# Kernel optimization log

Hardware: AMD Instinct MI355X
Metric: run time of the kernel (lower is better)

## Reference

```python
import jax, jax.numpy as jnp
import numpy as np

T, B, H, IN = 2048, 4096, 51, 2

def setup_inputs() -> dict:
    key = jax.random.key(0)
    ks = jax.random.split(key, 12)
    s = 1.0 / np.sqrt(H)
    u = lambda k, shape: jax.random.uniform(k, shape, jnp.float32, -s, s)
    return {
        "input": jax.random.normal(ks[0], (T, B, IN), jnp.float32),
        "W_ih1": u(ks[1], (4 * H, IN)),
        "W_hh1": u(ks[2], (4 * H, H)),
        "b_ih1": u(ks[3], (4 * H,)),
        "b_hh1": u(ks[4], (4 * H,)),
        "W_ih2": u(ks[5], (4 * H, H)),
        "W_hh2": u(ks[6], (4 * H, H)),
        "b_ih2": u(ks[7], (4 * H,)),
        "b_hh2": u(ks[8], (4 * H,)),
        "W_lin": u(ks[9], (1, H)),
        "b_lin": u(ks[10], (1,)),
    }

def _lstm_cell(x, h, c, W_ih, W_hh, b_ih, b_hh):
    # PyTorch LSTMCell gate order: input, forget, cell(g), output
    gates = x @ W_ih.T + b_ih + h @ W_hh.T + b_hh  # [B, 4H]
    i, f, g, o = jnp.split(gates, 4, axis=-1)
    c_new = jax.nn.sigmoid(f) * c + jax.nn.sigmoid(i) * jnp.tanh(g)
    h_new = jax.nn.sigmoid(o) * jnp.tanh(c_new)
    return h_new, c_new

def reference(input, W_ih1, W_hh1, b_ih1, b_hh1, W_ih2, W_hh2, b_ih2, b_hh2, W_lin, b_lin):
    Bsz = input.shape[1]
    z = jnp.zeros((Bsz, H), input.dtype)

    def step(carry, x_t):
        h1, c1, h2, c2 = carry
        h1, c1 = _lstm_cell(x_t, h1, c1, W_ih1, W_hh1, b_ih1, b_hh1)
        h2, c2 = _lstm_cell(h1, h2, c2, W_ih2, W_hh2, b_ih2, b_hh2)
        out = h2 @ W_lin.T + b_lin  # [B, 1]
        return (h1, c1, h2, c2), out[:, 0]

    _, outs = jax.lax.scan(step, (z, z, z, z), input)  # outs: [T, B]
    return outs.T  # [B, T] == torch.stack(outputs, 1).squeeze(2)
```

## Files before the change

### kernel.cpp

```cpp
#include <hip/hip_runtime.h>

namespace {
constexpr int T    = 2048;
constexpr int Bsz  = 4096;
constexpr int H    = 51;
constexpr int H4   = 204;
constexpr int NB   = 16;
constexpr int BLK  = 1024;
constexpr int GRID = Bsz / NB;
constexpr float SCI = -1.44269504f;
constexpr float SCG = -2.88539008f;
}

typedef float    f32x4 __attribute__((ext_vector_type(4)));
typedef _Float16 f16x8 __attribute__((ext_vector_type(8)));
typedef unsigned short u16;

__device__ __forceinline__ float RCP(float x)  { return __builtin_amdgcn_rcpf(x); }
__device__ __forceinline__ float EXP2(float x) { return __builtin_amdgcn_exp2f(x); }

__device__ __forceinline__ float lstm_act(float Gi, float Gf, float Gg, float Go, float& c) {
  float ei = EXP2(Gi);
  float ef = EXP2(Gf);
  float eo = EXP2(Go);
  float eg = EXP2(-fabsf(Gg));
  float pi = 1.0f + ei, pf = 1.0f + ef, pg = 1.0f + eg;
  float tg = copysignf(1.0f - eg, -Gg);
  float pig = pi * pg;
  float num = fmaf(c, pig, tg * pf);
  c = num * RCP(pig * pf);
  float ec = EXP2(SCG * fabsf(c));
  float tc = copysignf(1.0f - ec, c);
  return tc * RCP((1.0f + eo) * (1.0f + ec));
}


__global__ __launch_bounds__(BLK, 4) void lstm2_v5(
    const float* __restrict__ x,
    const float* __restrict__ Wih1, const float* __restrict__ Whh1,
    const float* __restrict__ bih1, const float* __restrict__ bhh1,
    const float* __restrict__ Wih2, const float* __restrict__ Whh2,
    const float* __restrict__ bih2, const float* __restrict__ bhh2,
    const float* __restrict__ Wlin, const float* __restrict__ blin,
    float* __restrict__ out) {
  __shared__ __align__(16) float  SW[H4 * H];
  __shared__ __align__(16) u16    PL[4096];
  __shared__ __align__(16) float2 XB[2][32][16];
  __shared__ __align__(16) float  OB[2][16][33];

  const int tid  = threadIdx.x;
  const int lane = tid & 63;
  const int wid  = tid >> 6;
  const int a    = lane & 15;
  const int q    = lane >> 4;
  const int b0   = blockIdx.x * NB;
  const int lt   = tid - 768;

  const int  l1t    = (wid <= 12) ? wid : -1;
  const int  l2t    = (wid < 12) ? wid : ((wid == 13) ? 12 : -1);
  const bool isHead = (wid == 14);
  const bool isXinj = (wid == 15);

  f16x8 wA1[2];
  f16x8 wA2[4];
  f16x8 hA[2][2];

  for (int i = tid; i < H4 * H; i += BLK) SW[i] = Whh1[i];
  __syncthreads();
  if (l1t >= 0) {
    const int  rp   = 16 * l1t + a;
    const bool vld  = (rp < H4);
    const int  gate = rp & 3;
    const int  wrow = gate * H + (rp >> 2);
    const float sc  = (gate == 2) ? SCG : SCI;
#pragma unroll
    for (int sp = 0; sp < 2; ++sp)
#pragma unroll
      for (int j = 0; j < 8; ++j) {
        const int k = 32 * sp + 16 * (j >> 2) + 4 * q + (j & 3);
        float val = 0.f;
        if (vld) {
          if (k < H)           val = SW[wrow * H + k];
          else if (k == H)     val = Wih1[wrow * 2 + 0];
          else if (k == H + 1) val = Wih1[wrow * 2 + 1];
          else if (k == H + 2) val = bih1[wrow] + bhh1[wrow];
        }
        wA1[sp][j] = (_Float16)(val * sc);
      }
  }
  __syncthreads();
  for (int i = tid; i < H4 * H; i += BLK) SW[i] = Wih2[i];
  __syncthreads();
  if (l2t >= 0) {
    const int  rp   = 16 * l2t + a;
    const bool vld  = (rp < H4);
    const int  gate = rp & 3;
    const int  wrow = gate * H + (rp >> 2);
    const float sc  = (gate == 2) ? SCG : SCI;
#pragma unroll
    for (int sp = 0; sp < 2; ++sp)
#pragma unroll
      for (int j = 0; j < 8; ++j) {
        const int k = 32 * sp + 16 * (j >> 2) + 4 * q + (j & 3);
        float val = 0.f;
        if (vld) {
          if (k < H)           val = SW[wrow * H + k];
          else if (k == H + 2) val = bih2[wrow] + bhh2[wrow];
        }
        wA2[sp][j] = (_Float16)(val * sc);
      }
  }
  __syncthreads();
  for (int i = tid; i < H4 * H; i += BLK) SW[i] = Whh2[i];
  __syncthreads();
  if (l2t >= 0) {
    const int  rp   = 16 * l2t + a;
    const bool vld  = (rp < H4);
    const int  gate = rp & 3;
    const int  wrow = gate * H + (rp >> 2);
    const float sc  = (gate == 2) ? SCG : SCI;
#pragma unroll
    for (int sp = 2; sp < 4; ++sp)
#pragma unroll
      for (int j = 0; j < 8; ++j) {
        const int kp = 32 * (sp - 2) + 16 * (j >> 2) + 4 * q + (j & 3);
        float val = (vld && kp < H) ? SW[wrow * H + kp] * sc : 0.f;
        wA2[sp][j] = (_Float16)val;
      }
  }
  if (isHead) {
#pragma unroll
    for (int sp = 0; sp < 2; ++sp)
#pragma unroll
      for (int j = 0; j < 8; ++j) {
        const int kp = 32 * sp + 16 * (j >> 2) + 4 * q + (j & 3);
        float val = 0.f;
        if (a == 0) {
          if (kp < H)           val = Wlin[kp];
          else if (kp == H + 2) val = blin[0];
        }
        const _Float16 hi = (_Float16)val;
        hA[sp][0][j] = hi;
        hA[sp][1][j] = (_Float16)(val - (float)hi);
      }
  }

  __syncthreads();
  for (int i = tid; i < 4096; i += BLK) PL[i] = 0;
  __syncthreads();
  if (tid < 16) {
#pragma unroll
    for (int buf = 0; buf < 2; ++buf) {
      PL[(buf * 4 + 1) * 512 + (tid + 16) * 8 + 5] = 0x3C00;
      PL[(buf * 4 + 3) * 512 + (tid + 16) * 8 + 5] = 0x3C00;
    }
  }
  if (lt >= 0) {
    const int st = lt >> 3, bc = (lt & 7) * 2;
    *(float4*)&XB[0][st][bc] = *(const float4*)(x + ((size_t)st * Bsz + b0 + bc) * 2);
  }
  __syncthreads();
  if (isXinj && lane < 32) {
    const int bb = lane & 15, f = lane >> 4;
    const float xv = ((const float*)&XB[0][0][0])[bb * 2 + f];
    const int idx = 512 + ((f == 0) ? bb * 8 + 7 : (bb + 16) * 8 + 4);
    *(_Float16*)&PL[idx] = (_Float16)xv;
  }
  __syncthreads();

  int wbase1 = 0, wbase2 = 0;
  bool uval1 = false, uval2 = false;
  if (l1t >= 0) {
    const int u = 4 * l1t + q; uval1 = (u < H);
    const int spl = u >> 5, kl = u & 31;
    wbase1 = spl * 512 + (a + 16 * ((kl >> 2) & 3)) * 8 + ((kl & 3) + 4 * (kl >> 4));
  }
  if (l2t >= 0) {
    const int u = 4 * l2t + q; uval2 = (u < H);
    const int spl = u >> 5, kl = u & 31;
    wbase2 = 1024 + spl * 512 + (a + 16 * ((kl >> 2) & 3)) * 8 + ((kl & 3) + 4 * (kl >> 4));
  }

  float c1 = 0.f, c2 = 0.f;
  float4 xcr = {0.f, 0.f, 0.f, 0.f};

  for (int s = 0; s < T + 3; ++s) {
    const int pb   = (s & 1) * 2048;
    const int nbuf = 2048 - pb;

    f16x8 bh0, bh1, bh2, bh3;
    if (l1t >= 0 || l2t >= 0) {
      bh0 = *(const f16x8*)&PL[pb + lane * 8];
      bh1 = *(const f16x8*)&PL[pb + 512 + lane * 8];
    }
    if (l2t >= 0 || isHead) {
      bh2 = *(const f16x8*)&PL[pb + 1024 + lane * 8];
      bh3 = *(const f16x8*)&PL[pb + 1536 + lane * 8];
    }

    if (lt >= 0) {
      const int ph = s & 31;
      if (ph == 0) {
        if (s + 32 < T) {
          const int st = lt >> 3, bc = (lt & 7) * 2;
          xcr = *(const float4*)(x + ((size_t)(s + 32 + st) * Bsz + b0 + bc) * 2);
        }
      } else if (ph == 1) {
        if (s + 31 < T) {
          const int buf = ((s >> 5) + 1) & 1;
          const int st = lt >> 3, bc = (lt & 7) * 2;
          *(float4*)&XB[buf][st][bc] = xcr;
        }
      } else if (ph == 2 && s >= 34) {
        const int f = (s - 34) >> 5;
        const int row = lt >> 4, c0 = (lt & 15) * 2;
        const float2 v = *(const float2*)&OB[f & 1][row][c0];
        *(float2*)(out + (size_t)(b0 + row) * T + f * 32 + c0) = v;
      }
    }

    f32x4 d1, d2;
    if (l1t >= 0) {
      f32x4 acc = {0.f, 0.f, 0.f, 0.f};
      acc = __builtin_amdgcn_mfma_f32_16x16x32_f16(wA1[0], bh0, acc, 0, 0, 0);
      acc = __builtin_amdgcn_mfma_f32_16x16x32_f16(wA1[1], bh1, acc, 0, 0, 0);
      d1 = acc;
    }
    if (l2t >= 0) {
      f32x4 acc = {0.f, 0.f, 0.f, 0.f};
      acc = __builtin_amdgcn_mfma_f32_16x16x32_f16(wA2[0], bh0, acc, 0, 0, 0);
      acc = __builtin_amdgcn_mfma_f32_16x16x32_f16(wA2[1], bh1, acc, 0, 0, 0);
      acc = __builtin_amdgcn_mfma_f32_16x16x32_f16(wA2[2], bh2, acc, 0, 0, 0);
      acc = __builtin_amdgcn_mfma_f32_16x16x32_f16(wA2[3], bh3, acc, 0, 0, 0);
      d2 = acc;
    }

    if (l1t >= 0 && s < T) {
      const float h1 = lstm_act(d1[0], d1[1], d1[2], d1[3], c1);
      if (uval1) *(_Float16*)&PL[nbuf + wbase1] = (_Float16)h1;
    }
    if (l2t >= 0 && s >= 1 && s <= T) {
      const float h2 = lstm_act(d2[0], d2[1], d2[2], d2[3], c2);
      if (uval2) *(_Float16*)&PL[nbuf + wbase2] = (_Float16)h2;
    }

    if (isHead) {
      f32x4 dh = {0.f, 0.f, 0.f, 0.f};
      dh = __builtin_amdgcn_mfma_f32_16x16x32_f16(hA[0][0], bh2, dh, 0, 0, 0);
      dh = __builtin_amdgcn_mfma_f32_16x16x32_f16(hA[0][1], bh2, dh, 0, 0, 0);
      dh = __builtin_amdgcn_mfma_f32_16x16x32_f16(hA[1][0], bh3, dh, 0, 0, 0);
      dh = __builtin_amdgcn_mfma_f32_16x16x32_f16(hA[1][1], bh3, dh, 0, 0, 0);
      if (s >= 2 && s - 2 < T && lane < 16)
        OB[((s - 2) >> 5) & 1][lane][(s - 2) & 31] = dh[0];
    }
    if (isXinj && lane < 32 && s + 1 < T) {
      const int bb = lane & 15, f = lane >> 4;
      const int st = (s + 1) & 31, cb = ((s + 1) >> 5) & 1;
      const float xv = ((const float*)&XB[cb][st][0])[bb * 2 + f];
      const int idx = nbuf + 512 + ((f == 0) ? bb * 8 + 7 : (bb + 16) * 8 + 4);
      *(_Float16*)&PL[idx] = (_Float16)xv;
    }
    __syncthreads();
  }
}

extern "C" void kernel_launch(void* const* d_in, const int* in_sizes, int n_in,
                              void* d_out, int out_size, void* d_ws, size_t ws_size,
                              hipStream_t stream) {
  (void)in_sizes; (void)n_in; (void)d_ws; (void)ws_size; (void)out_size;
  const float* x    = (const float*)d_in[0];
  const float* Wih1 = (const float*)d_in[1];
  const float* Whh1 = (const float*)d_in[2];
  const float* bih1 = (const float*)d_in[3];
  const float* bhh1 = (const float*)d_in[4];
  const float* Wih2 = (const float*)d_in[5];
  const float* Whh2 = (const float*)d_in[6];
  const float* bih2 = (const float*)d_in[7];
  const float* bhh2 = (const float*)d_in[8];
  const float* Wlin = (const float*)d_in[9];
  const float* blin = (const float*)d_in[10];
  float* out = (float*)d_out;

  hipLaunchKernelGGL(lstm2_v5, dim3(GRID), dim3(BLK), 0, stream,
                     x, Wih1, Whh1, bih1, bhh1, Wih2, Whh2, bih2, bhh2,
                     Wlin, blin, out);
}
```

Baseline: 1.360 ms.

## Halve batch per block and pack two gate tiles per wave with DPP select

Each block now handles 8 batch rows with 512 threads and 8 waves instead of 16 rows with 1024 threads. Each wave computes two 16-row gate tiles and uses a DPP row select to merge the valid 8-column halves. The head projection, x staging and output writeback move into one special wave, and the head drops its fp16 hi/lo split to a single fp16 weight. Role assignment is rotated per block to balance MFMA load across SIMDs. This doubles the grid and MFMA work per useful output column, trading denser per-step barriers for more redundant matrix work and slightly lower head precision.

```diff
diff --git a/kernel.cpp b/kernel.cpp
--- a/kernel.cpp
+++ b/kernel.cpp
@@ -5,8 +5,8 @@
 constexpr int Bsz  = 4096;
 constexpr int H    = 51;
 constexpr int H4   = 204;
-constexpr int NB   = 16;
-constexpr int BLK  = 1024;
+constexpr int NB   = 8;
+constexpr int BLK  = 512;
 constexpr int GRID = Bsz / NB;
 constexpr float SCI = -1.44269504f;
 constexpr float SCG = -2.88539008f;
@@ -34,8 +34,13 @@
   return tc * RCP((1.0f + eo) * (1.0f + ec));
 }
 
-
-__global__ __launch_bounds__(BLK, 4) void lstm2_v5(
+__device__ __forceinline__ float dpp_sel(float dA, float dB) {
+  return __uint_as_float((unsigned)__builtin_amdgcn_update_dpp(
+      (int)__float_as_uint(dA), (int)__float_as_uint(dB), 0x118, 0xf, 0xf, false));
+}
+
+
+__global__ __launch_bounds__(BLK, 4) void lstm2_v6(
     const float* __restrict__ x,
     const float* __restrict__ Wih1, const float* __restrict__ Whh1,
     const float* __restrict__ bih1, const float* __restrict__ bhh1,
@@ -45,8 +50,8 @@
     float* __restrict__ out) {
   __shared__ __align__(16) float  SW[H4 * H];
   __shared__ __align__(16) u16    PL[4096];
-  __shared__ __align__(16) float2 XB[2][32][16];
-  __shared__ __align__(16) float  OB[2][16][33];
+  __shared__ __align__(16) float4 XB4[2][32][4];
+  __shared__ __align__(16) float  OB[2][8][36];
 
   const int tid  = threadIdx.x;
   const int lane = tid & 63;
@@ -54,81 +59,94 @@
   const int a    = lane & 15;
   const int q    = lane >> 4;
   const int b0   = blockIdx.x * NB;
-  const int lt   = tid - 768;
-
-  const int  l1t    = (wid <= 12) ? wid : -1;
-  const int  l2t    = (wid < 12) ? wid : ((wid == 13) ? 12 : -1);
-  const bool isHead = (wid == 14);
-  const bool isXinj = (wid == 15);
-
-  f16x8 wA1[2];
-  f16x8 wA2[4];
-  f16x8 hA[2][2];
+
+  const int role = (wid + ((blockIdx.x & 1) << 1)) & 7;
+  int l1A = -1, l1B = -1, l2A = -1, l2B = -1;
+  bool isSpec = false;
+  if (role < 6)       { l1A = 2 * role; l1B = l1A + 1; l2A = l1A; l2B = l1B; }
+  else if (role == 6) { l1A = 12; }
+  else                { l2A = 12; isSpec = true; }
+
+  f16x8 wA1[2][2];
+  f16x8 wA2[2][4];
+  f16x8 hA[2];
 
   for (int i = tid; i < H4 * H; i += BLK) SW[i] = Whh1[i];
   __syncthreads();
-  if (l1t >= 0) {
-    const int  rp   = 16 * l1t + a;
-    const bool vld  = (rp < H4);
-    const int  gate = rp & 3;
-    const int  wrow = gate * H + (rp >> 2);
-    const float sc  = (gate == 2) ? SCG : SCI;
-#pragma unroll
-    for (int sp = 0; sp < 2; ++sp)
-#pragma unroll
-      for (int j = 0; j < 8; ++j) {
-        const int k = 32 * sp + 16 * (j >> 2) + 4 * q + (j & 3);
-        float val = 0.f;
-        if (vld) {
-          if (k < H)           val = SW[wrow * H + k];
-          else if (k == H)     val = Wih1[wrow * 2 + 0];
-          else if (k == H + 1) val = Wih1[wrow * 2 + 1];
-          else if (k == H + 2) val = bih1[wrow] + bhh1[wrow];
-        }
-        wA1[sp][j] = (_Float16)(val * sc);
-      }
+#pragma unroll
+  for (int ti = 0; ti < 2; ++ti) {
+    const int t = ti ? l1B : l1A;
+    if (t >= 0) {
+      const int  rp   = 16 * t + a;
+      const bool vld  = (rp < H4);
+      const int  gate = rp & 3;
+      const int  wrow = gate * H + (rp >> 2);
+      const float sc  = (gate == 2) ? SCG : SCI;
+#pragma unroll
+      for (int sp = 0; sp < 2; ++sp)
+#pragma unroll
+        for (int j = 0; j < 8; ++j) {
+          const int k = 32 * sp + 16 * (j >> 2) + 4 * q + (j & 3);
+          float val = 0.f;
+          if (vld) {
+            if (k < H)           val = SW[wrow * H + k];
+            else if (k == H)     val = Wih1[wrow * 2 + 0];
+            else if (k == H + 1) val = Wih1[wrow * 2 + 1];
+            else if (k == H + 2) val = bih1[wrow] + bhh1[wrow];
+          }
+          wA1[ti][sp][j] = (_Float16)(val * sc);
+        }
+    }
   }
   __syncthreads();
   for (int i = tid; i < H4 * H; i += BLK) SW[i] = Wih2[i];
   __syncthreads();
-  if (l2t >= 0) {
-    const int  rp   = 16 * l2t + a;
-    const bool vld  = (rp < H4);
-    const int  gate = rp & 3;
-    const int  wrow = gate * H + (rp >> 2);
-    const float sc  = (gate == 2) ? SCG : SCI;
-#pragma unroll
-    for (int sp = 0; sp < 2; ++sp)
-#pragma unroll
-      for (int j = 0; j < 8; ++j) {
-        const int k = 32 * sp + 16 * (j >> 2) + 4 * q + (j & 3);
-        float val = 0.f;
-        if (vld) {
-          if (k < H)           val = SW[wrow * H + k];
-          else if (k == H + 2) val = bih2[wrow] + bhh2[wrow];
-        }
-        wA2[sp][j] = (_Float16)(val * sc);
-      }
+#pragma unroll
+  for (int ti = 0; ti < 2; ++ti) {
+    const int t = ti ? l2B : l2A;
+    if (t >= 0) {
+      const int  rp   = 16 * t + a;
+      const bool vld  = (rp < H4);
+      const int  gate = rp & 3;
+      const int  wrow = gate * H + (rp >> 2);
+      const float sc  = (gate == 2) ? SCG : SCI;
+#pragma unroll
+      for (int sp = 0; sp < 2; ++sp)
+#pragma unroll
+        for (int j = 0; j < 8; ++j) {
+          const int k = 32 * sp + 16 * (j >> 2) + 4 * q + (j & 3);
+          float val = 0.f;
+          if (vld) {
+            if (k < H)           val = SW[wrow * H + k];
+            else if (k == H + 2) val = bih2[wrow] + bhh2[wrow];
+          }
+          wA2[ti][sp][j] = (_Float16)(val * sc);
+        }
+    }
   }
   __syncthreads();
   for (int i = tid; i < H4 * H; i += BLK) SW[i] = Whh2[i];
   __syncthreads();
-  if (l2t >= 0) {
-    const int  rp   = 16 * l2t + a;
-    const bool vld  = (rp < H4);
-    const int  gate = rp & 3;
-    const int  wrow = gate * H + (rp >> 2);
-    const float sc  = (gate == 2) ? SCG : SCI;
-#pragma unroll
-    for (int sp = 2; sp < 4; ++sp)
-#pragma unroll
-      for (int j = 0; j < 8; ++j) {
-        const int kp = 32 * (sp - 2) + 16 * (j >> 2) + 4 * q + (j & 3);
-        float val = (vld && kp < H) ? SW[wrow * H + kp] * sc : 0.f;
-        wA2[sp][j] = (_Float16)val;
-      }
-  }
-  if (isHead) {
+#pragma unroll
+  for (int ti = 0; ti < 2; ++ti) {
+    const int t = ti ? l2B : l2A;
+    if (t >= 0) {
+      const int  rp   = 16 * t + a;
+      const bool vld  = (rp < H4);
+      const int  gate = rp & 3;
+      const int  wrow = gate * H + (rp >> 2);
+      const float sc  = (gate == 2) ? SCG : SCI;
+#pragma unroll
+      for (int sp = 2; sp < 4; ++sp)
+#pragma unroll
+        for (int j = 0; j < 8; ++j) {
+          const int kp = 32 * (sp - 2) + 16 * (j >> 2) + 4 * q + (j & 3);
+          float val = (vld && kp < H) ? SW[wrow * H + kp] * sc : 0.f;
+          wA2[ti][sp][j] = (_Float16)val;
+        }
+    }
+  }
+  if (isSpec) {
 #pragma unroll
     for (int sp = 0; sp < 2; ++sp)
 #pragma unroll
@@ -139,14 +157,16 @@
           if (kp < H)           val = Wlin[kp];
           else if (kp == H + 2) val = blin[0];
         }
-        const _Float16 hi = (_Float16)val;
-        hA[sp][0][j] = hi;
-        hA[sp][1][j] = (_Float16)(val - (float)hi);
+        hA[sp][j] = (_Float16)val;
       }
   }
 
   __syncthreads();
   for (int i = tid; i < 4096; i += BLK) PL[i] = 0;
+  if (tid < 128) {
+    const int st = tid >> 2, v4 = tid & 3;
+    XB4[0][st][v4] = *(const float4*)(x + ((size_t)st * Bsz + b0) * 2 + v4 * 4);
+  }
   __syncthreads();
   if (tid < 16) {
 #pragma unroll
@@ -155,110 +175,142 @@
       PL[(buf * 4 + 3) * 512 + (tid + 16) * 8 + 5] = 0x3C00;
     }
   }
-  if (lt >= 0) {
-    const int st = lt >> 3, bc = (lt & 7) * 2;
-    *(float4*)&XB[0][st][bc] = *(const float4*)(x + ((size_t)st * Bsz + b0 + bc) * 2);
-  }
-  __syncthreads();
-  if (isXinj && lane < 32) {
-    const int bb = lane & 15, f = lane >> 4;
-    const float xv = ((const float*)&XB[0][0][0])[bb * 2 + f];
+  __syncthreads();
+  if (isSpec && lane < 16) {
+    const int bb = lane & 7, f = (lane >> 3) & 1;
+    const float xv = ((const float*)&XB4[0][0][0])[bb * 2 + f];
     const int idx = 512 + ((f == 0) ? bb * 8 + 7 : (bb + 16) * 8 + 4);
     *(_Float16*)&PL[idx] = (_Float16)xv;
   }
   __syncthreads();
 
-  int wbase1 = 0, wbase2 = 0;
+  int widx1 = 0, widx2 = 0;
   bool uval1 = false, uval2 = false;
-  if (l1t >= 0) {
-    const int u = 4 * l1t + q; uval1 = (u < H);
-    const int spl = u >> 5, kl = u & 31;
-    wbase1 = spl * 512 + (a + 16 * ((kl >> 2) & 3)) * 8 + ((kl & 3) + 4 * (kl >> 4));
-  }
-  if (l2t >= 0) {
-    const int u = 4 * l2t + q; uval2 = (u < H);
-    const int spl = u >> 5, kl = u & 31;
-    wbase2 = 1024 + spl * 512 + (a + 16 * ((kl >> 2) & 3)) * 8 + ((kl & 3) + 4 * (kl >> 4));
+  {
+    const int tt = (a < 8) ? l1A : l1B;
+    if (tt >= 0) {
+      const int u = 4 * tt + q;
+      if (u < H) {
+        uval1 = true;
+        const int spl = u >> 5, kl = u & 31;
+        widx1 = spl * 512 + ((a & 7) + 16 * ((kl >> 2) & 3)) * 8 + ((kl & 3) + 4 * (kl >> 4));
+      }
+    }
+  }
+  {
+    const int tt = (a < 8) ? l2A : l2B;
+    if (tt >= 0) {
+      const int u = 4 * tt + q;
+      if (u < H) {
+        uval2 = true;
+        const int spl = u >> 5, kl = u & 31;
+        widx2 = 1024 + spl * 512 + ((a & 7) + 16 * ((kl >> 2) & 3)) * 8 + ((kl & 3) + 4 * (kl >> 4));
+      }
+    }
   }
 
   float c1 = 0.f, c2 = 0.f;
-  float4 xcr = {0.f, 0.f, 0.f, 0.f};
+  float4 xcr0 = {0.f, 0.f, 0.f, 0.f}, xcr1 = {0.f, 0.f, 0.f, 0.f};
 
   for (int s = 0; s < T + 3; ++s) {
     const int pb   = (s & 1) * 2048;
     const int nbuf = 2048 - pb;
 
     f16x8 bh0, bh1, bh2, bh3;
-    if (l1t >= 0 || l2t >= 0) {
+    if (l1A >= 0 || l2A >= 0) {
       bh0 = *(const f16x8*)&PL[pb + lane * 8];
       bh1 = *(const f16x8*)&PL[pb + 512 + lane * 8];
     }
-    if (l2t >= 0 || isHead) {
+    if (l2A >= 0) {
       bh2 = *(const f16x8*)&PL[pb + 1024 + lane * 8];
       bh3 = *(const f16x8*)&PL[pb + 1536 + lane * 8];
     }
 
-    if (lt >= 0) {
+    if (isSpec) {
       const int ph = s & 31;
       if (ph == 0) {
         if (s + 32 < T) {
-          const int st = lt >> 3, bc = (lt & 7) * 2;
-          xcr = *(const float4*)(x + ((size_t)(s + 32 + st) * Bsz + b0 + bc) * 2);
+          const int st = lane >> 2, v4 = lane & 3;
+          xcr0 = *(const float4*)(x + ((size_t)(s + 32 + st) * Bsz + b0) * 2 + v4 * 4);
+          xcr1 = *(const float4*)(x + ((size_t)(s + 48 + st) * Bsz + b0) * 2 + v4 * 4);
         }
       } else if (ph == 1) {
         if (s + 31 < T) {
           const int buf = ((s >> 5) + 1) & 1;
-          const int st = lt >> 3, bc = (lt & 7) * 2;
-          *(float4*)&XB[buf][st][bc] = xcr;
+          const int st = lane >> 2, v4 = lane & 3;
+          XB4[buf][st][v4]      = xcr0;
+          XB4[buf][16 + st][v4] = xcr1;
         }
       } else if (ph == 2 && s >= 34) {
         const int f = (s - 34) >> 5;
-        const int row = lt >> 4, c0 = (lt & 15) * 2;
-        const float2 v = *(const float2*)&OB[f & 1][row][c0];
-        *(float2*)(out + (size_t)(b0 + row) * T + f * 32 + c0) = v;
-      }
-    }
-
-    f32x4 d1, d2;
-    if (l1t >= 0) {
+        const int row = lane >> 3, c4 = (lane & 7) * 4;
+        const float4 v = *(const float4*)&OB[f & 1][row][c4];
+        *(float4*)(out + (size_t)(b0 + row) * T + f * 32 + c4) = v;
+      }
+    }
+
+    f32x4 dA1, dB1, dA2, dB2;
+    if (l1A >= 0) {
       f32x4 acc = {0.f, 0.f, 0.f, 0.f};
-      acc = __builtin_amdgcn_mfma_f32_16x16x32_f16(wA1[0], bh0, acc, 0, 0, 0);
-      acc = __builtin_amdgcn_mfma_f32_16x16x32_f16(wA1[1], bh1, acc, 0, 0, 0);
-      d1 = acc;
-    }
-    if (l2t >= 0) {
+      acc = __builtin_amdgcn_mfma_f32_16x16x32_f16(wA1[0][0], bh0, acc, 0, 0, 0);
+      acc = __builtin_amdgcn_mfma_f32_16x16x32_f16(wA1[0][1], bh1, acc, 0, 0, 0);
+      dA1 = acc;
+      if (l1B >= 0) {
+        f32x4 ac2 = {0.f, 0.f, 0.f, 0.f};
+        ac2 = __builtin_amdgcn_mfma_f32_16x16x32_f16(wA1[1][0], bh0, ac2, 0, 0, 0);
+        ac2 = __builtin_amdgcn_mfma_f32_16x16x32_f16(wA1[1][1], bh1, ac2, 0, 0, 0);
+        dB1 = ac2;
+      }
+    }
+    if (l2A >= 0) {
       f32x4 acc = {0.f, 0.f, 0.f, 0.f};
-      acc = __builtin_amdgcn_mfma_f32_16x16x32_f16(wA2[0], bh0, acc, 0, 0, 0);
-      acc = __builtin_amdgcn_mfma_f32_16x16x32_f16(wA2[1], bh1, acc, 0, 0, 0);
-      acc = __builtin_amdgcn_mfma_f32_16x16x32_f16(wA2[2], bh2, acc, 0, 0, 0);
-      acc = __builtin_amdgcn_mfma_f32_16x16x32_f16(wA2[3], bh3, acc, 0, 0, 0);
-      d2 = acc;
-    }
-
-    if (l1t >= 0 && s < T) {
-      const float h1 = lstm_act(d1[0], d1[1], d1[2], d1[3], c1);
-      if (uval1) *(_Float16*)&PL[nbuf + wbase1] = (_Float16)h1;
-    }
-    if (l2t >= 0 && s >= 1 && s <= T) {
-      const float h2 = lstm_act(d2[0], d2[1], d2[2], d2[3], c2);
-      if (uval2) *(_Float16*)&PL[nbuf + wbase2] = (_Float16)h2;
-    }
-
-    if (isHead) {
+      acc = __builtin_amdgcn_mfma_f32_16x16x32_f16(wA2[0][0], bh0, acc, 0, 0, 0);
+      acc = __builtin_amdgcn_mfma_f32_16x16x32_f16(wA2[0][1], bh1, acc, 0, 0, 0);
+      acc = __builtin_amdgcn_mfma_f32_16x16x32_f16(wA2[0][2], bh2, acc, 0, 0, 0);
+      acc = __builtin_amdgcn_mfma_f32_16x16x32_f16(wA2[0][3], bh3, acc, 0, 0, 0);
+      dA2 = acc;
+      if (l2B >= 0) {
+        f32x4 ac2 = {0.f, 0.f, 0.f, 0.f};
+        ac2 = __builtin_amdgcn_mfma_f32_16x16x32_f16(wA2[1][0], bh0, ac2, 0, 0, 0);
+        ac2 = __builtin_amdgcn_mfma_f32_16x16x32_f16(wA2[1][1], bh1, ac2, 0, 0, 0);
+        ac2 = __builtin_amdgcn_mfma_f32_16x16x32_f16(wA2[1][2], bh2, ac2, 0, 0, 0);
+        ac2 = __builtin_amdgcn_mfma_f32_16x16x32_f16(wA2[1][3], bh3, ac2, 0, 0, 0);
+        dB2 = ac2;
+      }
+    }
+
+    if (l1A >= 0 && s < T) {
+      float g0, g1, g2, g3;
+      if (l1B >= 0) {
+        g0 = dpp_sel(dA1[0], dB1[0]); g1 = dpp_sel(dA1[1], dB1[1]);
+        g2 = dpp_sel(dA1[2], dB1[2]); g3 = dpp_sel(dA1[3], dB1[3]);
+      } else { g0 = dA1[0]; g1 = dA1[1]; g2 = dA1[2]; g3 = dA1[3]; }
+      const float h1 = lstm_act(g0, g1, g2, g3, c1);
+      if (uval1) *(_Float16*)&PL[nbuf + widx1] = (_Float16)h1;
+    }
+    if (l2A >= 0 && s >= 1 && s <= T) {
+      float g0, g1, g2, g3;
+      if (l2B >= 0) {
+        g0 = dpp_sel(dA2[0], dB2[0]); g1 = dpp_sel(dA2[1], dB2[1]);
+        g2 = dpp_sel(dA2[2], dB2[2]); g3 = dpp_sel(dA2[3], dB2[3]);
+      } else { g0 = dA2[0]; g1 = dA2[1]; g2 = dA2[2]; g3 = dA2[3]; }
+      const float h2 = lstm_act(g0, g1, g2, g3, c2);
+      if (uval2) *(_Float16*)&PL[nbuf + widx2] = (_Float16)h2;
+    }
+
+    if (isSpec) {
       f32x4 dh = {0.f, 0.f, 0.f, 0.f};
-      dh = __builtin_amdgcn_mfma_f32_16x16x32_f16(hA[0][0], bh2, dh, 0, 0, 0);
-      dh = __builtin_amdgcn_mfma_f32_16x16x32_f16(hA[0][1], bh2, dh, 0, 0, 0);
-      dh = __builtin_amdgcn_mfma_f32_16x16x32_f16(hA[1][0], bh3, dh, 0, 0, 0);
-      dh = __builtin_amdgcn_mfma_f32_16x16x32_f16(hA[1][1], bh3, dh, 0, 0, 0);
-      if (s >= 2 && s - 2 < T && lane < 16)
+      dh = __builtin_amdgcn_mfma_f32_16x16x32_f16(hA[0], bh2, dh, 0, 0, 0);
+      dh = __builtin_amdgcn_mfma_f32_16x16x32_f16(hA[1], bh3, dh, 0, 0, 0);
+      if (s >= 2 && s - 2 < T && lane < 8)
         OB[((s - 2) >> 5) & 1][lane][(s - 2) & 31] = dh[0];
-    }
-    if (isXinj && lane < 32 && s + 1 < T) {
-      const int bb = lane & 15, f = lane >> 4;
-      const int st = (s + 1) & 31, cb = ((s + 1) >> 5) & 1;
-      const float xv = ((const float*)&XB[cb][st][0])[bb * 2 + f];
-      const int idx = nbuf + 512 + ((f == 0) ? bb * 8 + 7 : (bb + 16) * 8 + 4);
-      *(_Float16*)&PL[idx] = (_Float16)xv;
+      if (lane < 16 && s + 1 < T) {
+        const int bb = lane & 7, f = (lane >> 3) & 1;
+        const int st = (s + 1) & 31, cb = ((s + 1) >> 5) & 1;
+        const float xv = ((const float*)&XB4[cb][st][0])[bb * 2 + f];
+        const int idx = nbuf + 512 + ((f == 0) ? bb * 8 + 7 : (bb + 16) * 8 + 4);
+        *(_Float16*)&PL[idx] = (_Float16)xv;
+      }
     }
     __syncthreads();
   }
@@ -281,7 +333,7 @@
   const float* blin = (const float*)d_in[10];
   float* out = (float*)d_out;
 
-  hipLaunchKernelGGL(lstm2_v5, dim3(GRID), dim3(BLK), 0, stream,
+  hipLaunchKernelGGL(lstm2_v6, dim3(GRID), dim3(BLK), 0, stream,
                      x, Wih1, Whh1, bih1, bhh1, Wih2, Whh2, bih2, bhh2,
                      Wlin, blin, out);
 }
```

Measured after the change: 2.012 ms. 48.0% more time.
